# Kernel tuning notes

Hardware: AMD Instinct MI355X
Metric: run time of the kernel (lower is better)

## Reference

```python
import jax, jax.numpy as jnp
import numpy as np

D = 512
H = 8
HD = D // H
EPS = 1e-6


def layer_norm(x, a, b):
    # torch: std is unbiased (ddof=1); note division by (std + eps), not sqrt(var+eps)
    mean = x.mean(-1, keepdims=True)
    std = jnp.sqrt(x.var(-1, ddof=1, keepdims=True))
    return a * (x - mean) / (std + EPS) + b


def setup_inputs() -> dict:
    key = jax.random.key(0)
    ks = jax.random.split(key, 8)
    x = jax.random.normal(ks[0], (4, 2048, D), dtype=jnp.float32)
    s = 0.02
    return {
        "x": x,
        "ln1_a": jnp.ones((D,), jnp.float32),
        "ln1_b": jnp.zeros((D,), jnp.float32),
        "ln2_a": jnp.ones((D,), jnp.float32),
        "ln2_b": jnp.zeros((D,), jnp.float32),
        "wq": jax.random.normal(ks[1], (D, D), jnp.float32) * s,  # [out, in] torch layout
        "wk": jax.random.normal(ks[2], (D, D), jnp.float32) * s,
        "wv": jax.random.normal(ks[3], (D, D), jnp.float32) * s,
        "wo": jax.random.normal(ks[4], (D, D), jnp.float32) * s,
        "w1": jax.random.normal(ks[5], (D, D), jnp.float32) * s,  # MLP hidden == dim
        "b1": jnp.zeros((D,), jnp.float32),
        "w2": jax.random.normal(ks[6], (D, D), jnp.float32) * s,
        "b2": jnp.zeros((D,), jnp.float32),
    }


def reference(x, ln1_a, ln1_b, ln2_a, ln2_b, wq, wk, wv, wo, w1, b1, w2, b2):
    B, S, _ = x.shape
    xn = layer_norm(x, ln1_a, ln1_b)
    # attention (non-causal, dropout=identity in eval)
    q = (xn @ wq.T).reshape(B, S, H, HD)
    k = (xn @ wk.T).reshape(B, S, H, HD)
    v = (xn @ wv.T).reshape(B, S, H, HD)
    scores = jnp.einsum("bshd,bthd->bhst", q, k) / jnp.sqrt(jnp.float32(HD))
    probs = jax.nn.softmax(scores.astype(jnp.float32), axis=-1).astype(q.dtype)
    attn = jnp.einsum("bhst,bthd->bshd", probs, v).reshape(B, S, D)
    h = xn + attn @ wo.T
    # MLP
    hn = layer_norm(h, ln2_a, ln2_b)
    ffn = jax.nn.relu(hn @ w1.T + b1) @ w2.T + b2
    return h + ffn
```

## Files before the change

kernel.cpp:

```cpp
#include <hip/hip_runtime.h>


typedef short s16x8 __attribute__((ext_vector_type(8)));
typedef float f32x4 __attribute__((ext_vector_type(4)));
typedef unsigned short u16;
typedef u16 u16x4 __attribute__((ext_vector_type(4)));

__device__ __forceinline__ u16 f2b(float f) {
  union { float f; unsigned u; } c; c.f = f;
  return (u16)((c.u + 0x7FFFu + ((c.u >> 16) & 1u)) >> 16);
}

__device__ __forceinline__ f32x4 mfma16(s16x8 a, s16x8 b, f32x4 c) {
  return __builtin_amdgcn_mfma_f32_16x16x32_bf16(a, b, c, 0, 0, 0);
}

__device__ __forceinline__ void gload_lds16(const u16* g, u16* l) {
  __builtin_amdgcn_global_load_lds(
      (const __attribute__((address_space(1))) unsigned*)g,
      (__attribute__((address_space(3))) unsigned*)l, 16, 0, 0);
}

__global__ __launch_bounds__(256) void cast_w(
    const float* __restrict__ s0, const float* __restrict__ s1,
    const float* __restrict__ s2, const float* __restrict__ s3,
    const float* __restrict__ s4, const float* __restrict__ s5,
    u16* __restrict__ dst)
{
  int i = blockIdx.x * 256 + threadIdx.x;
  const float* s;
  switch (blockIdx.y) {
    case 0: s = s0; break; case 1: s = s1; break; case 2: s = s2; break;
    case 3: s = s3; break; case 4: s = s4; break; default: s = s5; break;
  }
  float4 v = ((const float4*)s)[i];
  u16x4 o; o.x = f2b(v.x); o.y = f2b(v.y); o.z = f2b(v.z); o.w = f2b(v.w);
  *(u16x4*)(dst + (size_t)blockIdx.y * 262144 + (size_t)i * 4) = o;
}

template<int OF, int OB>
__global__ __launch_bounds__(256) void ln_kernel(
    const float* __restrict__ x, const float* __restrict__ ga,
    const float* __restrict__ gbv, float* __restrict__ yf, u16* __restrict__ yb)
{
  int row = blockIdx.x * 4 + (threadIdx.x >> 6);
  int lane = threadIdx.x & 63;
  size_t base = (size_t)row * 512 + lane * 8;
  const float4* xr = (const float4*)(x + base);
  float4 v0 = xr[0], v1 = xr[1];
  float s  = v0.x + v0.y + v0.z + v0.w + v1.x + v1.y + v1.z + v1.w;
  float ss = v0.x*v0.x + v0.y*v0.y + v0.z*v0.z + v0.w*v0.w
           + v1.x*v1.x + v1.y*v1.y + v1.z*v1.z + v1.w*v1.w;
  #pragma unroll
  for (int m = 1; m < 64; m <<= 1) { s += __shfl_xor(s, m); ss += __shfl_xor(ss, m); }
  float mean = s * (1.0f / 512.0f);
  float var  = fmaxf((ss - 512.0f * mean * mean) * (1.0f / 511.0f), 0.0f);
  float inv  = 1.0f / (sqrtf(var) + 1e-6f);
  const float4* ap = (const float4*)(ga + lane * 8);
  const float4* bp = (const float4*)(gbv + lane * 8);
  float4 a0 = ap[0], a1 = ap[1], b0 = bp[0], b1 = bp[1];
  float4 y0, y1;
  y0.x = (v0.x-mean)*inv*a0.x + b0.x;  y0.y = (v0.y-mean)*inv*a0.y + b0.y;
  y0.z = (v0.z-mean)*inv*a0.z + b0.z;  y0.w = (v0.w-mean)*inv*a0.w + b0.w;
  y1.x = (v1.x-mean)*inv*a1.x + b1.x;  y1.y = (v1.y-mean)*inv*a1.y + b1.y;
  y1.z = (v1.z-mean)*inv*a1.z + b1.z;  y1.w = (v1.w-mean)*inv*a1.w + b1.w;
  if (OF) { float4* o = (float4*)(yf + base); o[0] = y0; o[1] = y1; }
  if (OB) {
    union { s16x8 v; u16 u[8]; } pk;
    pk.u[0]=f2b(y0.x); pk.u[1]=f2b(y0.y); pk.u[2]=f2b(y0.z); pk.u[3]=f2b(y0.w);
    pk.u[4]=f2b(y1.x); pk.u[5]=f2b(y1.y); pk.u[6]=f2b(y1.z); pk.u[7]=f2b(y1.w);
    *(s16x8*)(yb + base) = pk.v;
  }
}

template<int MODE>
__global__ __launch_bounds__(256) void gemm128(
    const u16* __restrict__ A, const u16* __restrict__ W,
    const float* __restrict__ bias, const float* __restrict__ resid,
    float* __restrict__ outf, u16* __restrict__ outb,
    u16* __restrict__ outb2, u16* __restrict__ outb3, float qscale)
{
  __shared__ u16 als[2][128 * 32];
  __shared__ u16 bls[2][128 * 32];
  int t = threadIdx.x, lane = t & 63, w = t >> 6;
  int l15 = lane & 15, g = lane >> 4;
  int wr = w >> 1, wc = w & 1;
  int mbase = blockIdx.x * 128, nbase = blockIdx.y * 128;

  int r0 = t >> 2, cs = (t & 3) ^ ((r0 >> 1) & 3);
  size_t offA0 = (size_t)(mbase + r0) * 512 + cs * 8;
  size_t offA1 = (size_t)(mbase + r0 + 64) * 512 + cs * 8;
  size_t offB0 = (size_t)(nbase + r0) * 512 + cs * 8;
  size_t offB1 = (size_t)(nbase + r0 + 64) * 512 + cs * 8;

  #define GSTAGE(buf, k0) do {                                    \
    gload_lds16(A + (k0) + offA0, &als[buf][(w * 64) * 8]);       \
    gload_lds16(A + (k0) + offA1, &als[buf][(256 + w * 64) * 8]); \
    gload_lds16(W + (k0) + offB0, &bls[buf][(w * 64) * 8]);       \
    gload_lds16(W + (k0) + offB1, &bls[buf][(256 + w * 64) * 8]); \
  } while (0)

  int ar[4], br[4];
  #pragma unroll
  for (int i = 0; i < 4; ++i) {
    int rA = wr * 64 + i * 16 + l15;
    ar[i] = rA * 32 + ((g ^ ((rA >> 1) & 3)) << 3);
    int rB = wc * 64 + i * 16 + l15;
    br[i] = rB * 32 + ((g ^ ((rB >> 1) & 3)) << 3);
  }

  f32x4 zero = {0.0f, 0.0f, 0.0f, 0.0f};
  f32x4 acc[4][4];
  #pragma unroll
  for (int mi = 0; mi < 4; ++mi)
    #pragma unroll
    for (int ni = 0; ni < 4; ++ni) acc[mi][ni] = zero;

  GSTAGE(0, 0);
  __syncthreads();
  int cur = 0;
  for (int kk = 0; kk < 16; ++kk) {
    if (kk < 15) GSTAGE(cur ^ 1, (kk + 1) * 32);
    s16x8 af[4], bfr[4];
    #pragma unroll
    for (int i = 0; i < 4; ++i) {
      af[i]  = *(const s16x8*)&als[cur][ar[i]];
      bfr[i] = *(const s16x8*)&bls[cur][br[i]];
    }
    #pragma unroll
    for (int mi = 0; mi < 4; ++mi)
      #pragma unroll
      for (int ni = 0; ni < 4; ++ni)
        acc[mi][ni] = mfma16(af[mi], bfr[ni], acc[mi][ni]);
    __syncthreads();
    cur ^= 1;
  }
  #undef GSTAGE

  #pragma unroll
  for (int ni = 0; ni < 4; ++ni) {
    int n = nbase + wc * 64 + ni * 16 + l15;
    float bv = (MODE & 1) ? bias[n] : 0.0f;
    #pragma unroll
    for (int mi = 0; mi < 4; ++mi) {
      #pragma unroll
      for (int r = 0; r < 4; ++r) {
        int m = mbase + wr * 64 + mi * 16 + 4 * g + r;
        float v = acc[mi][ni][r] + bv;
        if (MODE & 2) v = fmaxf(v, 0.0f);
        if (MODE & 4) v += resid[(size_t)m * 512 + n];
        if (MODE & 8) outf[(size_t)m * 512 + n] = v;
        if (MODE & 16) outb[(size_t)m * 512 + n] = f2b(v);
        if (MODE & 64) {
          if (nbase < 512) {
            outb[(size_t)m * 512 + n] = f2b(v * qscale);
          } else if (nbase < 1024) {
            outb2[(size_t)m * 512 + (n - 512)] = f2b(v);
          } else {
            int nn = n - 1024;
            int sidx = m & 2047;
            int jj = sidx & 31, lo4 = jj & 15, b5 = jj >> 4;
            int pos = ((lo4 >> 2) << 3) + ((lo4 & 3) << 1) + b5;
            outb3[(size_t)((m >> 11) * 512 + nn) * 2048 + (sidx & ~31) + pos] = f2b(v);
          }
        }
      }
    }
  }
}

__global__ __launch_bounds__(256) void attn_kernel(
    const u16* __restrict__ q, const u16* __restrict__ k,
    const u16* __restrict__ vt, u16* __restrict__ o)
{
  __shared__ u16 kls[2][64 * 64];
  __shared__ u16 vls[2][64 * 64];
  int t = threadIdx.x, lane = t & 63, w = t >> 6;
  int l15 = lane & 15, g = lane >> 4;
  int sw = l15 & 7;
  int lrow = lane >> 3;
  int lchunk = (lane & 7) ^ (lrow & 7);
  int fid = blockIdx.x + 32 * blockIdx.y;
  int xcd = fid & 7, rest = fid >> 3;
  int bh = xcd * 4 + (rest & 3);
  int qt = rest >> 2;
  int bb = bh >> 3, h = bh & 7;
  int qbase = qt * 128 + w * 32;

  const u16* qp = q + (size_t)(bb * 2048 + qbase + l15) * 512 + h * 64 + g * 8;
  s16x8 qf0a = *(const s16x8*)qp;
  s16x8 qf1a = *(const s16x8*)(qp + 32);
  s16x8 qf0b = *(const s16x8*)(qp + 16 * 512);
  s16x8 qf1b = *(const s16x8*)(qp + 16 * 512 + 32);
  f32x4 zero = {0.0f, 0.0f, 0.0f, 0.0f};
  f32x4 oacc[2][4];
  #pragma unroll
  for (int qg = 0; qg < 2; ++qg)
    #pragma unroll
    for (int nf = 0; nf < 4; ++nf) oacc[qg][nf] = zero;
  float lsum[2] = {0.0f, 0.0f};
  const u16* kb0 = k + (size_t)(bb * 2048) * 512 + h * 64;
  const u16* vb0 = vt + (size_t)((bb * 8 + h) * 64) * 2048;

  #define STAGE(nb, tt) do {                                                  \
    int r0 = w * 16 + lrow;                                                   \
    const u16* ks0 = kb0 + (size_t)((tt) * 64 + r0) * 512 + lchunk * 8;       \
    const u16* vs0 = vb0 + (size_t)r0 * 2048 + (tt) * 64 + lchunk * 8;        \
    gload_lds16(ks0, &kls[nb][(w * 16) * 64]);                                \
    gload_lds16(ks0 + (size_t)8 * 512, &kls[nb][(w * 16 + 8) * 64]);          \
    gload_lds16(vs0, &vls[nb][(w * 16) * 64]);                                \
    gload_lds16(vs0 + (size_t)8 * 2048, &vls[nb][(w * 16 + 8) * 64]);         \
  } while (0)

  STAGE(0, 0);
  __syncthreads();
  int cur = 0;

  for (int kt = 0; kt < 32; ++kt) {
    if (kt + 1 < 32) STAGE(cur ^ 1, kt + 1);
    f32x4 s[2][4];
    #pragma unroll
    for (int kg = 0; kg < 4; ++kg) {
      int rb = (kg * 16 + l15) * 64;
      s16x8 ka = *(const s16x8*)&kls[cur][rb + ((g ^ sw) << 3)];
      s16x8 kc = *(const s16x8*)&kls[cur][rb + (((4 + g) ^ sw) << 3)];
      s[0][kg] = mfma16(ka, qf0a, zero);
      s[0][kg] = mfma16(kc, qf1a, s[0][kg]);
      s[1][kg] = mfma16(ka, qf0b, zero);
      s[1][kg] = mfma16(kc, qf1b, s[1][kg]);
    }
    union { s16x8 v8; unsigned u32v[4]; } pk[2][2];
    #pragma unroll
    for (int qg = 0; qg < 2; ++qg) {
      #pragma unroll
      for (int b2 = 0; b2 < 2; ++b2) {
        #pragma unroll
        for (int r = 0; r < 4; ++r) {
          float p0 = __builtin_amdgcn_exp2f(s[qg][2 * b2][r]);
          float p1 = __builtin_amdgcn_exp2f(s[qg][2 * b2 + 1][r]);
          lsum[qg] += p0 + p1;
          union { float f; unsigned u; } a, b;
          a.f = p0; b.f = p1;
          pk[qg][b2].u32v[r] = __builtin_amdgcn_perm(b.u, a.u, 0x07060302u);
        }
      }
    }
    #pragma unroll
    for (int b2 = 0; b2 < 2; ++b2) {
      #pragma unroll
      for (int nf = 0; nf < 4; ++nf) {
        s16x8 vf = *(const s16x8*)
            &vls[cur][(nf * 16 + l15) * 64 + ((((b2 << 2) | g) ^ sw) << 3)];
        oacc[0][nf] = mfma16(pk[0][b2].v8, vf, oacc[0][nf]);
        oacc[1][nf] = mfma16(pk[1][b2].v8, vf, oacc[1][nf]);
      }
    }
    __syncthreads();
    cur ^= 1;
  }
  #undef STAGE

  #pragma unroll
  for (int qg = 0; qg < 2; ++qg) {
    float ls = lsum[qg];
    ls += __shfl_xor(ls, 16);
    ls += __shfl_xor(ls, 32);
    float linv = 1.0f / ls;
    size_t obase = (size_t)(bb * 2048 + qbase + qg * 16 + 4 * g) * 512
                 + h * 64 + l15;
    #pragma unroll
    for (int r = 0; r < 4; ++r) {
      float lr = __shfl(linv, 4 * g + r);
      #pragma unroll
      for (int nf = 0; nf < 4; ++nf)
        o[obase + (size_t)r * 512 + nf * 16] = f2b(oacc[qg][nf][r] * lr);
    }
  }
}

extern "C" void kernel_launch(void* const* d_in, const int* in_sizes, int n_in,
                              void* d_out, int out_size, void* d_ws, size_t ws_size,
                              hipStream_t stream)
{
  const float* x     = (const float*)d_in[0];
  const float* ln1_a = (const float*)d_in[1];
  const float* ln1_b = (const float*)d_in[2];
  const float* ln2_a = (const float*)d_in[3];
  const float* ln2_b = (const float*)d_in[4];
  const float* wq = (const float*)d_in[5];
  const float* wk = (const float*)d_in[6];
  const float* wv = (const float*)d_in[7];
  const float* wo = (const float*)d_in[8];
  const float* w1 = (const float*)d_in[9];
  const float* b1 = (const float*)d_in[10];
  const float* w2 = (const float*)d_in[11];
  const float* b2 = (const float*)d_in[12];

  char* ws = (char*)d_ws;
  float* xn_f = (float*)(ws + (size_t)0);
  float* h_f  = (float*)(ws + ((size_t)16 << 20));
  u16* xn_b = (u16*)(ws + ((size_t)32 << 20));
  u16* q_b  = (u16*)(ws + ((size_t)40 << 20));
  u16* k_b  = (u16*)(ws + ((size_t)48 << 20));
  u16* vt_b = (u16*)(ws + ((size_t)56 << 20));
  u16* at_b = (u16*)(ws + ((size_t)64 << 20));
  u16* wb   = (u16*)(ws + ((size_t)72 << 20));
  u16 *wob = wb + 3*262144, *w1b = wb + 4 * 262144, *w2b = wb + 5 * 262144;
  u16* hn_b = q_b;
  u16* f_b  = at_b;

  dim3 blk(256);
  cast_w<<<dim3(256, 6), blk, 0, stream>>>(wq, wk, wv, wo, w1, w2, wb);
  ln_kernel<1, 1><<<dim3(2048), blk, 0, stream>>>(x, ln1_a, ln1_b, xn_f, xn_b);
  gemm128<64><<<dim3(64, 12), blk, 0, stream>>>(
      xn_b, wb, nullptr, nullptr, nullptr, q_b, k_b, vt_b, 0.18033688f);
  attn_kernel<<<dim3(32, 16), blk, 0, stream>>>(q_b, k_b, vt_b, at_b);
  gemm128<4 | 8><<<dim3(64, 4), blk, 0, stream>>>(
      at_b, wob, nullptr, xn_f, h_f, nullptr, nullptr, nullptr, 0.0f);
  ln_kernel<0, 1><<<dim3(2048), blk, 0, stream>>>(h_f, ln2_a, ln2_b, nullptr, hn_b);
  gemm128<1 | 2 | 16><<<dim3(64, 4), blk, 0, stream>>>(
      hn_b, w1b, b1, nullptr, nullptr, f_b, nullptr, nullptr, 0.0f);
  gemm128<1 | 4 | 8><<<dim3(64, 4), blk, 0, stream>>>(
      f_b, w2b, b2, h_f, (float*)d_out, nullptr, nullptr, nullptr, 0.0f);
}
```

Before: 137.8 us.

## Triple-buffer LDS staging in GEMM and attention with partial vmcnt waits

Both the GEMM and the attention kernel move from double to triple LDS buffering, keeping two tiles in flight. Each iteration waits only until the current tile's loads land (vmcnt(4)) and uses one barrier, instead of draining all loads before a full __syncthreads. This is meant to hide global-to-LDS latency better and drop one barrier per iteration, at the cost of 50% more LDS per block, which may reduce occupancy. It also relies on hand-written waitcnt values matching the compiler's order of memory operations.

```diff
diff --git a/kernel.cpp b/kernel.cpp
--- a/kernel.cpp
+++ b/kernel.cpp
@@ -80,8 +80,8 @@
     float* __restrict__ outf, u16* __restrict__ outb,
     u16* __restrict__ outb2, u16* __restrict__ outb3, float qscale)
 {
-  __shared__ u16 als[2][128 * 32];
-  __shared__ u16 bls[2][128 * 32];
+  __shared__ u16 als[3][128 * 32];
+  __shared__ u16 bls[3][128 * 32];
   int t = threadIdx.x, lane = t & 63, w = t >> 6;
   int l15 = lane & 15, g = lane >> 4;
   int wr = w >> 1, wc = w & 1;
@@ -117,23 +117,30 @@
     for (int ni = 0; ni < 4; ++ni) acc[mi][ni] = zero;
 
   GSTAGE(0, 0);
-  __syncthreads();
-  int cur = 0;
+  GSTAGE(1, 32);
+  int bi = 0;
   for (int kk = 0; kk < 16; ++kk) {
-    if (kk < 15) GSTAGE(cur ^ 1, (kk + 1) * 32);
+    if (kk < 15) asm volatile("s_waitcnt vmcnt(4)" ::: "memory");
+    else         asm volatile("s_waitcnt vmcnt(0)" ::: "memory");
+    __builtin_amdgcn_s_barrier();
+    if (kk + 2 < 16) {
+      int pi = bi + 2; if (pi >= 3) pi -= 3;
+      GSTAGE(pi, (kk + 2) * 32);
+    }
+    const u16* acur = als[bi];
+    const u16* bcur = bls[bi];
     s16x8 af[4], bfr[4];
     #pragma unroll
     for (int i = 0; i < 4; ++i) {
-      af[i]  = *(const s16x8*)&als[cur][ar[i]];
-      bfr[i] = *(const s16x8*)&bls[cur][br[i]];
+      af[i]  = *(const s16x8*)&acur[ar[i]];
+      bfr[i] = *(const s16x8*)&bcur[br[i]];
     }
     #pragma unroll
     for (int mi = 0; mi < 4; ++mi)
       #pragma unroll
       for (int ni = 0; ni < 4; ++ni)
         acc[mi][ni] = mfma16(af[mi], bfr[ni], acc[mi][ni]);
-    __syncthreads();
-    cur ^= 1;
+    bi = (bi == 2) ? 0 : bi + 1;
   }
   #undef GSTAGE
 
@@ -173,8 +180,8 @@
     const u16* __restrict__ q, const u16* __restrict__ k,
     const u16* __restrict__ vt, u16* __restrict__ o)
 {
-  __shared__ u16 kls[2][64 * 64];
-  __shared__ u16 vls[2][64 * 64];
+  __shared__ u16 kls[3][64 * 64];
+  __shared__ u16 vls[3][64 * 64];
   int t = threadIdx.x, lane = t & 63, w = t >> 6;
   int l15 = lane & 15, g = lane >> 4;
   int sw = l15 & 7;
@@ -203,9 +210,9 @@
   const u16* vb0 = vt + (size_t)((bb * 8 + h) * 64) * 2048;
 
   #define STAGE(nb, tt) do {                                                  \
-    int r0 = w * 16 + lrow;                                                   \
-    const u16* ks0 = kb0 + (size_t)((tt) * 64 + r0) * 512 + lchunk * 8;       \
-    const u16* vs0 = vb0 + (size_t)r0 * 2048 + (tt) * 64 + lchunk * 8;        \
+    int sr0 = w * 16 + lrow;                                                  \
+    const u16* ks0 = kb0 + (size_t)((tt) * 64 + sr0) * 512 + lchunk * 8;      \
+    const u16* vs0 = vb0 + (size_t)sr0 * 2048 + (tt) * 64 + lchunk * 8;       \
     gload_lds16(ks0, &kls[nb][(w * 16) * 64]);                                \
     gload_lds16(ks0 + (size_t)8 * 512, &kls[nb][(w * 16 + 8) * 64]);          \
     gload_lds16(vs0, &vls[nb][(w * 16) * 64]);                                \
@@ -213,17 +220,25 @@
   } while (0)
 
   STAGE(0, 0);
-  __syncthreads();
-  int cur = 0;
+  STAGE(1, 1);
+  int bi = 0;
 
   for (int kt = 0; kt < 32; ++kt) {
-    if (kt + 1 < 32) STAGE(cur ^ 1, kt + 1);
+    if (kt < 31) asm volatile("s_waitcnt vmcnt(4)" ::: "memory");
+    else         asm volatile("s_waitcnt vmcnt(0)" ::: "memory");
+    __builtin_amdgcn_s_barrier();
+    if (kt + 2 < 32) {
+      int pi = bi + 2; if (pi >= 3) pi -= 3;
+      STAGE(pi, kt + 2);
+    }
+    const u16* kcur = kls[bi];
+    const u16* vcur = vls[bi];
     f32x4 s[2][4];
     #pragma unroll
     for (int kg = 0; kg < 4; ++kg) {
       int rb = (kg * 16 + l15) * 64;
-      s16x8 ka = *(const s16x8*)&kls[cur][rb + ((g ^ sw) << 3)];
-      s16x8 kc = *(const s16x8*)&kls[cur][rb + (((4 + g) ^ sw) << 3)];
+      s16x8 ka = *(const s16x8*)&kcur[rb + ((g ^ sw) << 3)];
+      s16x8 kc = *(const s16x8*)&kcur[rb + (((4 + g) ^ sw) << 3)];
       s[0][kg] = mfma16(ka, qf0a, zero);
       s[0][kg] = mfma16(kc, qf1a, s[0][kg]);
       s[1][kg] = mfma16(ka, qf0b, zero);
@@ -250,13 +265,12 @@
       #pragma unroll
       for (int nf = 0; nf < 4; ++nf) {
         s16x8 vf = *(const s16x8*)
-            &vls[cur][(nf * 16 + l15) * 64 + ((((b2 << 2) | g) ^ sw) << 3)];
+            &vcur[(nf * 16 + l15) * 64 + ((((b2 << 2) | g) ^ sw) << 3)];
         oacc[0][nf] = mfma16(pk[0][b2].v8, vf, oacc[0][nf]);
         oacc[1][nf] = mfma16(pk[1][b2].v8, vf, oacc[1][nf]);
       }
     }
-    __syncthreads();
-    cur ^= 1;
+    bi = (bi == 2) ? 0 : bi + 1;
   }
   #undef STAGE
 
```

After: 144.8 us. 5.1% more time.

## Deepen attention K/V pipeline to four LDS buffers and software-pipeline QK^T

Applied to the files above, without the earlier changes.

Replaces the double-buffered K/V LDS staging with a four-slot ring that keeps three tiles in flight, using explicit vmcnt waits and one raw barrier per iteration instead of two __syncthreads. The QK^T MFMAs for the next tile are issued before the softmax and PV of the current tile, so exp work overlaps matrix-core work. The cost is twice the LDS footprint (64 KB per block), which can lower occupancy, and more score registers live at once.

```diff
diff --git a/kernel.cpp b/kernel.cpp
--- a/kernel.cpp
+++ b/kernel.cpp
@@ -173,8 +173,8 @@
     const u16* __restrict__ q, const u16* __restrict__ k,
     const u16* __restrict__ vt, u16* __restrict__ o)
 {
-  __shared__ u16 kls[2][64 * 64];
-  __shared__ u16 vls[2][64 * 64];
+  __shared__ u16 kls[4][64 * 64];
+  __shared__ u16 vls[4][64 * 64];
   int t = threadIdx.x, lane = t & 63, w = t >> 6;
   int l15 = lane & 15, g = lane >> 4;
   int sw = l15 & 7;
@@ -203,61 +203,88 @@
   const u16* vb0 = vt + (size_t)((bb * 8 + h) * 64) * 2048;
 
   #define STAGE(nb, tt) do {                                                  \
-    int r0 = w * 16 + lrow;                                                   \
-    const u16* ks0 = kb0 + (size_t)((tt) * 64 + r0) * 512 + lchunk * 8;       \
-    const u16* vs0 = vb0 + (size_t)r0 * 2048 + (tt) * 64 + lchunk * 8;        \
+    int sr0 = w * 16 + lrow;                                                  \
+    const u16* ks0 = kb0 + (size_t)((tt) * 64 + sr0) * 512 + lchunk * 8;      \
+    const u16* vs0 = vb0 + (size_t)sr0 * 2048 + (tt) * 64 + lchunk * 8;       \
     gload_lds16(ks0, &kls[nb][(w * 16) * 64]);                                \
     gload_lds16(ks0 + (size_t)8 * 512, &kls[nb][(w * 16 + 8) * 64]);          \
     gload_lds16(vs0, &vls[nb][(w * 16) * 64]);                                \
     gload_lds16(vs0 + (size_t)8 * 2048, &vls[nb][(w * 16 + 8) * 64]);         \
   } while (0)
 
+  #define QKT(kbuf, sdst) do {                                                \
+    _Pragma("unroll")                                                         \
+    for (int kg = 0; kg < 4; ++kg) {                                          \
+      int rb = (kg * 16 + l15) * 64;                                          \
+      s16x8 ka = *(const s16x8*)&(kbuf)[rb + ((g ^ sw) << 3)];                \
+      s16x8 kc = *(const s16x8*)&(kbuf)[rb + (((4 + g) ^ sw) << 3)];          \
+      sdst[0][kg] = mfma16(ka, qf0a, zero);                                   \
+      sdst[0][kg] = mfma16(kc, qf1a, sdst[0][kg]);                            \
+      sdst[1][kg] = mfma16(ka, qf0b, zero);                                   \
+      sdst[1][kg] = mfma16(kc, qf1b, sdst[1][kg]);                            \
+    }                                                                         \
+  } while (0)
+
+  #define SMAX(ssrc) do {                                                     \
+    _Pragma("unroll")                                                         \
+    for (int qg = 0; qg < 2; ++qg) {                                          \
+      _Pragma("unroll")                                                       \
+      for (int b2 = 0; b2 < 2; ++b2) {                                        \
+        _Pragma("unroll")                                                     \
+        for (int r = 0; r < 4; ++r) {                                         \
+          float p0 = __builtin_amdgcn_exp2f(ssrc[qg][2 * b2][r]);             \
+          float p1 = __builtin_amdgcn_exp2f(ssrc[qg][2 * b2 + 1][r]);         \
+          lsum[qg] += p0 + p1;                                                \
+          union { float f; unsigned u; } ua, ub;                              \
+          ua.f = p0; ub.f = p1;                                               \
+          pk[qg][b2].u32v[r] = __builtin_amdgcn_perm(ub.u, ua.u, 0x07060302u);\
+        }                                                                     \
+      }                                                                       \
+    }                                                                         \
+  } while (0)
+
+  #define PVC(vbuf) do {                                                      \
+    _Pragma("unroll")                                                         \
+    for (int b2 = 0; b2 < 2; ++b2) {                                          \
+      _Pragma("unroll")                                                       \
+      for (int nf = 0; nf < 4; ++nf) {                                        \
+        s16x8 vf = *(const s16x8*)                                            \
+            &(vbuf)[(nf * 16 + l15) * 64 + ((((b2 << 2) | g) ^ sw) << 3)];    \
+        oacc[0][nf] = mfma16(pk[0][b2].v8, vf, oacc[0][nf]);                  \
+        oacc[1][nf] = mfma16(pk[1][b2].v8, vf, oacc[1][nf]);                  \
+      }                                                                       \
+    }                                                                         \
+  } while (0)
+
+  typedef union { s16x8 v8; unsigned u32v[4]; } pku;
+
+  #define ITER(kt, scur, snxt) do {                                           \
+    if ((kt) < 30) asm volatile("s_waitcnt vmcnt(4)" ::: "memory");           \
+    else           asm volatile("s_waitcnt vmcnt(0)" ::: "memory");           \
+    __builtin_amdgcn_s_barrier();                                             \
+    if ((kt) + 3 < 32) STAGE(((kt) + 3) & 3, (kt) + 3);                       \
+    if ((kt) + 1 < 32) QKT(kls[((kt) + 1) & 3], snxt);                        \
+    pku pk[2][2];                                                             \
+    SMAX(scur);                                                               \
+    PVC(vls[(kt) & 3]);                                                       \
+  } while (0)
+
   STAGE(0, 0);
-  __syncthreads();
-  int cur = 0;
-
-  for (int kt = 0; kt < 32; ++kt) {
-    if (kt + 1 < 32) STAGE(cur ^ 1, kt + 1);
-    f32x4 s[2][4];
-    #pragma unroll
-    for (int kg = 0; kg < 4; ++kg) {
-      int rb = (kg * 16 + l15) * 64;
-      s16x8 ka = *(const s16x8*)&kls[cur][rb + ((g ^ sw) << 3)];
-      s16x8 kc = *(const s16x8*)&kls[cur][rb + (((4 + g) ^ sw) << 3)];
-      s[0][kg] = mfma16(ka, qf0a, zero);
-      s[0][kg] = mfma16(kc, qf1a, s[0][kg]);
-      s[1][kg] = mfma16(ka, qf0b, zero);
-      s[1][kg] = mfma16(kc, qf1b, s[1][kg]);
-    }
-    union { s16x8 v8; unsigned u32v[4]; } pk[2][2];
-    #pragma unroll
-    for (int qg = 0; qg < 2; ++qg) {
-      #pragma unroll
-      for (int b2 = 0; b2 < 2; ++b2) {
-        #pragma unroll
-        for (int r = 0; r < 4; ++r) {
-          float p0 = __builtin_amdgcn_exp2f(s[qg][2 * b2][r]);
-          float p1 = __builtin_amdgcn_exp2f(s[qg][2 * b2 + 1][r]);
-          lsum[qg] += p0 + p1;
-          union { float f; unsigned u; } a, b;
-          a.f = p0; b.f = p1;
-          pk[qg][b2].u32v[r] = __builtin_amdgcn_perm(b.u, a.u, 0x07060302u);
-        }
-      }
-    }
-    #pragma unroll
-    for (int b2 = 0; b2 < 2; ++b2) {
-      #pragma unroll
-      for (int nf = 0; nf < 4; ++nf) {
-        s16x8 vf = *(const s16x8*)
-            &vls[cur][(nf * 16 + l15) * 64 + ((((b2 << 2) | g) ^ sw) << 3)];
-        oacc[0][nf] = mfma16(pk[0][b2].v8, vf, oacc[0][nf]);
-        oacc[1][nf] = mfma16(pk[1][b2].v8, vf, oacc[1][nf]);
-      }
-    }
-    __syncthreads();
-    cur ^= 1;
-  }
+  STAGE(1, 1);
+  STAGE(2, 2);
+  asm volatile("s_waitcnt vmcnt(8)" ::: "memory");
+  __builtin_amdgcn_s_barrier();
+  f32x4 sA[2][4], sB[2][4];
+  QKT(kls[0], sA);
+
+  for (int k2 = 0; k2 < 32; k2 += 2) {
+    ITER(k2, sA, sB);
+    ITER(k2 + 1, sB, sA);
+  }
+  #undef ITER
+  #undef PVC
+  #undef SMAX
+  #undef QKT
   #undef STAGE
 
   #pragma unroll
```

Result: faster. 133.5 us (-3.1%).
